# Kernel tuning notes

Measured on AMD Instinct MI355X. Metric: run time of the kernel, lower is better.

## Reference

```python
import jax, jax.numpy as jnp
import numpy as np

N, E, G = 100_000, 1_200_000, 256
EPS = 1e-5

def _bn(a, g, b):
    # BatchNorm1d in training mode: biased batch statistics over dim 0
    mu = a.mean(0)
    var = ((a - mu) ** 2).mean(0)
    return (a - mu) * jax.lax.rsqrt(var + EPS) * g + b

def _cgconv(x, src, dst, ea, Wf, bf, Ws, bs, g, b):
    # PyG CGConv: z = [x_i, x_j, edge_attr]; m = sigmoid(lin_f(z)) * softplus(lin_s(z));
    # out = BN(scatter_add(m -> dst)) + x
    z = jnp.concatenate([x[dst], x[src], ea], axis=-1)      # [E, 2*64+1]
    m = jax.nn.sigmoid(z @ Wf + bf) * jax.nn.softplus(z @ Ws + bs)  # [E, 64]
    agg = jax.ops.segment_sum(m, dst, num_segments=x.shape[0])
    return _bn(agg, g, b) + x

def setup_inputs() -> dict:
    key = jax.random.key(0)
    ks = jax.random.split(key, 16)
    def w(k, shape, scale):
        return jax.random.normal(k, shape, jnp.float32) * scale
    inp = {
        "x": jax.random.normal(ks[0], (N, 12), jnp.float32),
        "edge_index": jax.random.randint(ks[1], (2, E), 0, N, jnp.int32),
        "edge_attr": jax.random.uniform(ks[2], (E, 1), dtype=jnp.float32),
        "batch": jnp.sort(jax.random.randint(ks[3], (N,), 0, G, jnp.int32)),
        "W_in": w(ks[4], (12, 64), 0.3), "b_in": jnp.zeros((64,), jnp.float32),
        "g0": jnp.ones((64,), jnp.float32), "beta0": jnp.zeros((64,), jnp.float32),
    }
    i = 5
    for l in (1, 2, 3):
        inp[f"Wf{l}"] = w(ks[i], (129, 64), 0.1)
        inp[f"bf{l}"] = jnp.zeros((64,), jnp.float32)
        inp[f"Ws{l}"] = w(ks[i + 1], (129, 64), 0.1)
        inp[f"bs{l}"] = jnp.zeros((64,), jnp.float32)
        inp[f"g{l}"] = jnp.ones((64,), jnp.float32)
        inp[f"bb{l}"] = jnp.zeros((64,), jnp.float32)
        i += 2
    inp["W1"] = w(ks[11], (64, 32), 0.15)
    inp["b1"] = jnp.zeros((32,), jnp.float32)
    inp["W2"] = w(ks[12], (32, 1), 0.2)
    inp["b2"] = jnp.zeros((1,), jnp.float32)
    return inp

def reference(x, edge_index, edge_attr, batch,
              W_in, b_in, g0, beta0,
              Wf1, bf1, Ws1, bs1, g1, bb1,
              Wf2, bf2, Ws2, bs2, g2, bb2,
              Wf3, bf3, Ws3, bs3, g3, bb3,
              W1, b1, W2, b2):
    src, dst = edge_index[0], edge_index[1]
    h = jax.nn.relu(_bn(x @ W_in + b_in, g0, beta0))
    h = jax.nn.relu(_cgconv(h, src, dst, edge_attr, Wf1, bf1, Ws1, bs1, g1, bb1))
    h = jax.nn.relu(_cgconv(h, src, dst, edge_attr, Wf2, bf2, Ws2, bs2, g2, bb2))
    h = _cgconv(h, src, dst, edge_attr, Wf3, bf3, Ws3, bs3, g3, bb3)
    # global_mean_pool
    s = jax.ops.segment_sum(h, batch, num_segments=G)
    c = jax.ops.segment_sum(jnp.ones((h.shape[0],), h.dtype), batch, num_segments=G)
    pooled = s / jnp.maximum(c, 1.0)[:, None]
    return jax.nn.relu(pooled @ W1 + b1) @ W2 + b2  # [G, 1]
```

## Files before the change

### kernel.cpp

```cpp
#include <hip/hip_runtime.h>
#include <math.h>

#define N_NODES 100000
#define N_EDGES 1200000
#define N_GRAPHS 256
#define CH 64
#define NC (N_NODES * CH)
#define EPS 1e-5f
#define LOG2E 1.4426950408889634f
#define LN2 0.6931471805599453f
#define EA_SCALE 32768.0f

#define SCAN_NB 98
#define ZSTRN 72
#define GTILES ((N_NODES + 63) / 64)
#define EA_BLOCKS 4096
#define NW (EA_BLOCKS * 4)
#define POOL_BLOCKS 256
#define WP2ROWS 64
#define CAP 48

#define NCOLORS 8
#define SC_BLOCKS 2048
#define NCHUNK (SC_BLOCKS / NCOLORS)
#define CSZ ((N_EDGES + NCHUNK - 1) / NCHUNK)
#define RNODES ((N_NODES + NCOLORS - 1) / NCOLORS)

#define EMB_BLOCKS 512
#define PREP_BLOCKS 192
#define PRE_BLOCKS (SC_BLOCKS + EMB_BLOCKS + PREP_BLOCKS)

typedef _Float16 half8 __attribute__((ext_vector_type(8)));
typedef _Float16 half2v __attribute__((ext_vector_type(2)));
typedef float floatx4 __attribute__((ext_vector_type(4)));

__device__ __forceinline__ int lbound(const int* __restrict__ a, int n, int v) {
    int lo = 0, hi = n;
    while (lo < hi) {
        int mid = (lo + hi) >> 1;
        if (a[mid] < v) lo = mid + 1; else hi = mid;
    }
    return lo;
}

__device__ __forceinline__ float gate2(float f2, float s2) {
    float ef = __builtin_amdgcn_exp2f(-f2);
    float sig = __builtin_amdgcn_rcpf(1.0f + ef);
    float es = __builtin_amdgcn_exp2f(-fabsf(s2));
    float sp = fmaxf(s2, 0.0f) + __builtin_amdgcn_logf(1.0f + es);
    return sig * sp;
}

__global__ void pre_kernel(const int* __restrict__ ei,
                           const float* __restrict__ ea,
                           int* __restrict__ rowptr,
                           unsigned* __restrict__ sef2,
                           const float* __restrict__ x,
                           const float* __restrict__ W,
                           const float* __restrict__ b,
                           _Float16* __restrict__ emb,
                           float* __restrict__ stats,
                           const float* __restrict__ Wf0, const float* __restrict__ Ws0,
                           const float* __restrict__ bf0, const float* __restrict__ bs0,
                           const float* __restrict__ Wf1, const float* __restrict__ Ws1,
                           const float* __restrict__ bf1, const float* __restrict__ bs1,
                           const float* __restrict__ Wf2, const float* __restrict__ Ws2,
                           const float* __restrict__ bf2, const float* __restrict__ bs2,
                           _Float16* __restrict__ WT2,
                           float* __restrict__ w128,
                           float* __restrict__ bias) {
    const int bid = blockIdx.x;
    if (bid < SC_BLOCKS) {
        const int j = bid & (NCOLORS - 1);
        const int k = bid >> 3;
        const int dlo = j * RNODES;
        const int dhi = min(N_NODES, dlo + RNODES);
        const int e0 = k * CSZ;
        const int e1 = min(N_EDGES, e0 + CSZ);
        for (int e = e0 + threadIdx.x; e < e1; e += 256) {
            int d = ei[N_EDGES + e];
            if (d >= dlo && d < dhi) {
                int slot = atomicAdd(&rowptr[d + 1], 1);
                if (slot < CAP) {
                    unsigned v = ((unsigned)ei[e] << 15) | (unsigned)(ea[e] * EA_SCALE);
                    sef2[(size_t)d * CAP + slot] = v;
                }
            }
        }
    } else if (bid < SC_BLOCKS + EMB_BLOCKS) {
        const int eb = bid - SC_BLOCKS;
        int c = threadIdx.x & 63;
        int sub = threadIdx.x >> 6;
        float s = 0.f, q = 0.f;
        for (int r = eb * 4 + sub; r < N_NODES; r += EMB_BLOCKS * 4) {
            const float* xr = x + r * 12;
            float acc = b[c];
#pragma unroll
            for (int k = 0; k < 12; ++k)
                acc = fmaf(xr[k], W[k * CH + c], acc);
            _Float16 h = (_Float16)acc;
            emb[(size_t)r * CH + c] = h;
            float hf = (float)h;
            s += hf;
            q = fmaf(hf, hf, q);
        }
        __shared__ float ls[4][64];
        __shared__ float lq[4][64];
        ls[sub][c] = s;
        lq[sub][c] = q;
        __syncthreads();
        if (sub == 0) {
            s = ls[0][c] + ls[1][c] + ls[2][c] + ls[3][c];
            q = lq[0][c] + lq[1][c] + lq[2][c] + lq[3][c];
            atomicAdd(&stats[c], s);
            atomicAdd(&stats[64 + c], q);
        }
    } else {
        int gid = (bid - SC_BLOCKS - EMB_BLOCKS) * 256 + threadIdx.x;
        int l = gid >> 14;
        int idx = gid & 16383;
        if (l >= 3) return;
        const float* Wf = (l == 0) ? Wf0 : (l == 1) ? Wf1 : Wf2;
        const float* Ws = (l == 0) ? Ws0 : (l == 1) ? Ws1 : Ws2;
        const float* bf = (l == 0) ? bf0 : (l == 1) ? bf1 : bf2;
        const float* bs = (l == 0) ? bs0 : (l == 1) ? bs1 : bs2;
        {
            int cc = idx >> 6;
            int k = idx & 63;
            float v;
            if (cc < 128) {
                int ch = cc >> 1;
                v = (cc & 1) ? Ws[k * 64 + ch] : Wf[k * 64 + ch];
            } else {
                int jj = cc - 128, ch = jj >> 1;
                v = (jj & 1) ? Ws[(64 + k) * 64 + ch] : Wf[(64 + k) * 64 + ch];
            }
            WT2[l * 16384 + idx] = (_Float16)(v * LOG2E);
        }
        if (idx < 128) {
            w128[l * 128 + idx] = ((idx < 64) ? Wf[128 * 64 + idx] : Ws[128 * 64 + (idx - 64)])
                                  * (LOG2E / EA_SCALE);
            bias[l * 128 + idx] = ((idx < 64) ? bf[idx] : bs[idx - 64]) * LOG2E;
        }
    }
}

__global__ void scanA_kernel(int* __restrict__ a, int* __restrict__ btot) {
    __shared__ int wsum[16];
    int t = threadIdx.x, lane = t & 63, w = t >> 6;
    int i = blockIdx.x * 1024 + t;
    int v = (i <= N_NODES) ? a[i] : 0;
    int s = v;
#pragma unroll
    for (int d = 1; d < 64; d <<= 1) {
        int o = __shfl_up(s, d);
        if (lane >= d) s += o;
    }
    if (lane == 63) wsum[w] = s;
    __syncthreads();
    if (w == 0) {
        int ws2 = (lane < 16) ? wsum[lane] : 0;
#pragma unroll
        for (int d = 1; d < 16; d <<= 1) {
            int o = __shfl_up(ws2, d);
            if (lane >= d) ws2 += o;
        }
        if (lane < 16) wsum[lane] = ws2;
    }
    __syncthreads();
    int off = (w > 0) ? wsum[w - 1] : 0;
    if (i <= N_NODES) a[i] = s + off;
    if (t == 0) btot[blockIdx.x] = wsum[15];
}

__global__ void scanB_kernel(int* __restrict__ btot) {
    int lane = threadIdx.x;
    int carry = 0;
    for (int base = 0; base < SCAN_NB; base += 64) {
        int i = base + lane;
        int v = (i < SCAN_NB) ? btot[i] : 0;
        int s = v;
#pragma unroll
        for (int d = 1; d < 64; d <<= 1) {
            int o = __shfl_up(s, d);
            if (lane >= d) s += o;
        }
        if (i < SCAN_NB) btot[i] = s + carry;
        carry += __shfl(s, 63);
    }
}

__global__ void scanC_kernel(int* __restrict__ a, const int* __restrict__ btot) {
    int i = blockIdx.x * 1024 + threadIdx.x;
    int off = (blockIdx.x > 0) ? btot[blockIdx.x - 1] : 0;
    if (i <= N_NODES) a[i] += off;
}

__global__ void wrange_kernel(const int* __restrict__ rowptr,
                              int* __restrict__ wrange) {
    int gid = blockIdx.x * blockDim.x + threadIdx.x;
    if (gid > NW) return;
    if (gid == NW) { wrange[NW] = N_NODES; return; }
    int e0t = (int)((long)gid * N_EDGES / NW);
    wrange[gid] = lbound(rowptr, N_NODES + 1, e0t);
}

template <bool RES, bool RED>
__global__ __launch_bounds__(256)
void node_gemm_kernel(const _Float16* __restrict__ ain,
                      const _Float16* __restrict__ res,
                      const float* __restrict__ stats,
                      const float* __restrict__ gamma,
                      const float* __restrict__ beta,
                      const _Float16* __restrict__ WT2,
                      _Float16* __restrict__ hout,
                      _Float16* __restrict__ pqrs) {
    __shared__ __align__(16) _Float16 As[64 * ZSTRN];
    __shared__ __align__(16) float ab[128];
    __shared__ float sw[128];
    const int t = threadIdx.x;
    const int lane = t & 63;
    const int w = t >> 6;
    const int l15 = lane & 15;
    const int quad = lane >> 4;

    if (RED) {
        if (t < 128) {
            float s = 0.f;
#pragma unroll 8
            for (int r = 0; r < WP2ROWS; ++r) s += stats[r * 128 + t];
            sw[t] = s;
        }
        __syncthreads();
    }
    if (t < 64) {
        float s0 = RED ? sw[t] : stats[t];
        float s1 = RED ? sw[64 + t] : stats[64 + t];
        float mean = s0 * (1.0f / (float)N_NODES);
        float var  = s1 * (1.0f / (float)N_NODES) - mean * mean;
        float inv  = rsqrtf(var + EPS);
        float A = gamma[t] * inv;
        ab[t] = A;
        ab[64 + t] = beta[t] - mean * A;
    }

    half8 bfr[4][2];
#pragma unroll
    for (int tt = 0; tt < 4; ++tt)
#pragma unroll
        for (int ks = 0; ks < 2; ++ks)
            bfr[tt][ks] = *(const half8*)(WT2 + (w * 64 + tt * 16 + l15) * 64 + ks * 32 + quad * 8);
    __syncthreads();

    const int base = blockIdx.x * 64;
    {
        const int e = t >> 2, q = t & 3;
        const int row = base + e;
        const bool valid = (row < N_NODES);
        const int crow = valid ? row : (N_NODES - 1);
        float af[16];
        {
            const _Float16* aph = ain + (size_t)crow * CH + q * 16;
            half8 h0 = *(const half8*)aph;
            half8 h1 = *(const half8*)(aph + 8);
#pragma unroll
            for (int j = 0; j < 8; ++j) { af[j] = (float)h0[j]; af[8 + j] = (float)h1[j]; }
        }
        float rf[16];
        if (RES) {
            const _Float16* rph = res + (size_t)crow * CH + q * 16;
            half8 r0 = *(const half8*)rph;
            half8 r1 = *(const half8*)(rph + 8);
#pragma unroll
            for (int j = 0; j < 8; ++j) { rf[j] = (float)r0[j]; rf[8 + j] = (float)r1[j]; }
        }
        float vv[16];
#pragma unroll
        for (int i = 0; i < 4; ++i) {
            float4 A4 = *(const float4*)(ab + q * 16 + i * 4);
            float4 B4 = *(const float4*)(ab + 64 + q * 16 + i * 4);
#pragma unroll
            for (int jj = 0; jj < 4; ++jj) {
                float Ax = (jj == 0) ? A4.x : (jj == 1) ? A4.y : (jj == 2) ? A4.z : A4.w;
                float Bx = (jj == 0) ? B4.x : (jj == 1) ? B4.y : (jj == 2) ? B4.z : B4.w;
                float r = RES ? rf[i * 4 + jj] : 0.f;
                vv[i * 4 + jj] = fmaxf(fmaf(af[i * 4 + jj], Ax, Bx) + r, 0.0f);
            }
        }
        half8 o0, o1;
#pragma unroll
        for (int j = 0; j < 8; ++j) { o0[j] = (_Float16)vv[j]; o1[j] = (_Float16)vv[8 + j]; }
        *(half8*)(As + e * ZSTRN + q * 16) = o0;
        *(half8*)(As + e * ZSTRN + q * 16 + 8) = o1;
        if (valid) {
            half8* hp = (half8*)(hout + (size_t)row * CH + q * 16);
            hp[0] = o0;
            hp[1] = o1;
        }
    }
    __syncthreads();

    floatx4 acc[4][4];
#pragma unroll
    for (int rt = 0; rt < 4; ++rt)
#pragma unroll
        for (int tt = 0; tt < 4; ++tt)
#pragma unroll
            for (int r = 0; r < 4; ++r) acc[rt][tt][r] = 0.f;

#pragma unroll
    for (int ks = 0; ks < 2; ++ks) {
#pragma unroll
        for (int rt = 0; rt < 4; ++rt) {
            half8 a = *(const half8*)(As + (rt * 16 + l15) * ZSTRN + ks * 32 + quad * 8);
#pragma unroll
            for (int tt = 0; tt < 4; ++tt)
                acc[rt][tt] = __builtin_amdgcn_mfma_f32_16x16x32_f16(a, bfr[tt][ks], acc[rt][tt], 0, 0, 0);
        }
    }

#pragma unroll
    for (int rt = 0; rt < 4; ++rt) {
#pragma unroll
        for (int r = 0; r < 4; ++r) {
            int row = base + rt * 16 + quad * 4 + r;
            if (row < N_NODES) {
#pragma unroll
                for (int tt = 0; tt < 4; ++tt)
                    pqrs[(size_t)row * 256 + w * 64 + tt * 16 + l15] = (_Float16)acc[rt][tt][r];
            }
        }
    }
}

__global__ __launch_bounds__(256)
void edge_agg_kernel(const _Float16* __restrict__ pqrs,
                     const unsigned* __restrict__ sef2,
                     const int* __restrict__ rowptr,
                     const int* __restrict__ wrange,
                     const float* __restrict__ w128,
                     const float* __restrict__ bias,
                     _Float16* __restrict__ agg,
                     float* __restrict__ wpart2) {
    const int lane = threadIdx.x & 63;
    const int w = threadIdx.x >> 6;
    const int gw = __builtin_amdgcn_readfirstlane(blockIdx.x * 4 + w);
    const float wfc = w128[lane], wsc = w128[64 + lane];
    const float bfc = bias[lane], bsc = bias[64 + lane];
    const half2v* __restrict__ prb = (const half2v*)pqrs;
    const half2v* __restrict__ qsb = (const half2v*)pqrs + 64;

    const int n0 = wrange[gw];
    const int n1 = wrange[gw + 1];

    float ssum = 0.f, sqsum = 0.f;
    if (n0 < n1) {
        half2v prn = prb[(size_t)n0 * 128 + lane];
        int rp1 = rowptr[n0];
        for (int n = n0; n < n1; ++n) {
            const int rp0 = rp1;
            rp1 = rowptr[n + 1];
            int deg = rp1 - rp0;
            if (deg > CAP) deg = CAP;
            const unsigned* sp = sef2 + (size_t)n * CAP;
            half2v pr = prn;
            {
                int np = (n + 1 < N_NODES) ? (n + 1) : (N_NODES - 1);
                prn = prb[(size_t)np * 128 + lane];
            }
            const float fb = (float)pr[0] + bfc;
            const float sb = (float)pr[1] + bsc;
            float acc0 = 0.f, acc1 = 0.f, acc2 = 0.f, acc3 = 0.f;
            int e = 0;
            for (; e + 8 <= deg; e += 8) {
                unsigned s0 = sp[e],     s1 = sp[e + 1], s2 = sp[e + 2], s3 = sp[e + 3];
                unsigned s4 = sp[e + 4], s5 = sp[e + 5], s6 = sp[e + 6], s7 = sp[e + 7];
                half2v q0 = qsb[(size_t)(s0 >> 15) * 128 + lane];
                half2v q1 = qsb[(size_t)(s1 >> 15) * 128 + lane];
                half2v q2 = qsb[(size_t)(s2 >> 15) * 128 + lane];
                half2v q3 = qsb[(size_t)(s3 >> 15) * 128 + lane];
                half2v q4 = qsb[(size_t)(s4 >> 15) * 128 + lane];
                half2v q5 = qsb[(size_t)(s5 >> 15) * 128 + lane];
                half2v q6 = qsb[(size_t)(s6 >> 15) * 128 + lane];
                half2v q7 = qsb[(size_t)(s7 >> 15) * 128 + lane];
                float ea0 = (float)(s0 & 32767u), ea1 = (float)(s1 & 32767u);
                float ea2 = (float)(s2 & 32767u), ea3 = (float)(s3 & 32767u);
                float ea4 = (float)(s4 & 32767u), ea5 = (float)(s5 & 32767u);
                float ea6 = (float)(s6 & 32767u), ea7 = (float)(s7 & 32767u);
                acc0 += gate2(fmaf(ea0, wfc, fb + (float)q0[0]), fmaf(ea0, wsc, sb + (float)q0[1]));
                acc1 += gate2(fmaf(ea1, wfc, fb + (float)q1[0]), fmaf(ea1, wsc, sb + (float)q1[1]));
                acc2 += gate2(fmaf(ea2, wfc, fb + (float)q2[0]), fmaf(ea2, wsc, sb + (float)q2[1]));
                acc3 += gate2(fmaf(ea3, wfc, fb + (float)q3[0]), fmaf(ea3, wsc, sb + (float)q3[1]));
                acc0 += gate2(fmaf(ea4, wfc, fb + (float)q4[0]), fmaf(ea4, wsc, sb + (float)q4[1]));
                acc1 += gate2(fmaf(ea5, wfc, fb + (float)q5[0]), fmaf(ea5, wsc, sb + (float)q5[1]));
                acc2 += gate2(fmaf(ea6, wfc, fb + (float)q6[0]), fmaf(ea6, wsc, sb + (float)q6[1]));
                acc3 += gate2(fmaf(ea7, wfc, fb + (float)q7[0]), fmaf(ea7, wsc, sb + (float)q7[1]));
            }
            if (e + 4 <= deg) {
                unsigned s0 = sp[e], s1 = sp[e + 1], s2 = sp[e + 2], s3 = sp[e + 3];
                half2v q0 = qsb[(size_t)(s0 >> 15) * 128 + lane];
                half2v q1 = qsb[(size_t)(s1 >> 15) * 128 + lane];
                half2v q2 = qsb[(size_t)(s2 >> 15) * 128 + lane];
                half2v q3 = qsb[(size_t)(s3 >> 15) * 128 + lane];
                float ea0 = (float)(s0 & 32767u), ea1 = (float)(s1 & 32767u);
                float ea2 = (float)(s2 & 32767u), ea3 = (float)(s3 & 32767u);
                acc0 += gate2(fmaf(ea0, wfc, fb + (float)q0[0]), fmaf(ea0, wsc, sb + (float)q0[1]));
                acc1 += gate2(fmaf(ea1, wfc, fb + (float)q1[0]), fmaf(ea1, wsc, sb + (float)q1[1]));
                acc2 += gate2(fmaf(ea2, wfc, fb + (float)q2[0]), fmaf(ea2, wsc, sb + (float)q2[1]));
                acc3 += gate2(fmaf(ea3, wfc, fb + (float)q3[0]), fmaf(ea3, wsc, sb + (float)q3[1]));
                e += 4;
            }
            for (; e < deg; ++e) {
                unsigned s0 = sp[e];
                half2v q0 = qsb[(size_t)(s0 >> 15) * 128 + lane];
                float ea0 = (float)(s0 & 32767u);
                acc0 += gate2(fmaf(ea0, wfc, fb + (float)q0[0]), fmaf(ea0, wsc, sb + (float)q0[1]));
            }
            _Float16 ah = (_Float16)(LN2 * ((acc0 + acc1) + (acc2 + acc3)));
            agg[(size_t)n * CH + lane] = ah;
            float acc = (float)ah;
            ssum += acc;
            sqsum = fmaf(acc, acc, sqsum);
        }
    }
    __shared__ float reds[4][128];
    reds[w][lane] = ssum;
    reds[w][64 + lane] = sqsum;
    __syncthreads();
    if (w == 0) {
        float a = reds[0][lane] + reds[1][lane] + reds[2][lane] + reds[3][lane];
        float b = reds[0][64 + lane] + reds[1][64 + lane] + reds[2][64 + lane] + reds[3][64 + lane];
        float* wp = wpart2 + (size_t)(blockIdx.x & (WP2ROWS - 1)) * 128;
        atomicAdd(&wp[lane], a);
        atomicAdd(&wp[64 + lane], b);
    }
}

__global__ __launch_bounds__(256)
void pool_bn_kernel(const _Float16* __restrict__ ain,
                    const _Float16* __restrict__ res,
                    const float* __restrict__ wp2,
                    const float* __restrict__ gamma,
                    const float* __restrict__ beta,
                    const int* __restrict__ batch,
                    float* __restrict__ pooled,
                    float* __restrict__ counts) {
    __shared__ float sw[128];
    __shared__ float ab[128];
    if (threadIdx.x < 128) {
        float s = 0.f;
#pragma unroll 8
        for (int r = 0; r < WP2ROWS; ++r) s += wp2[r * 128 + threadIdx.x];
        sw[threadIdx.x] = s;
    }
    __syncthreads();
    if (threadIdx.x < 64) {
        int t = threadIdx.x;
        float mean = sw[t] * (1.0f / (float)N_NODES);
        float var  = sw[64 + t] * (1.0f / (float)N_NODES) - mean * mean;
        float inv  = rsqrtf(var + EPS);
        float A = gamma[t] * inv;
        ab[t] = A;
        ab[64 + t] = beta[t] - mean * A;
    }
    __syncthreads();

    const int c = threadIdx.x & 63;
    const float A = ab[c], B = ab[64 + c];
    const int walker = blockIdx.x * 4 + (threadIdx.x >> 6);
    const int nwalk = POOL_BLOCKS * 4;
    const int chunk = (N_NODES + nwalk - 1) / nwalk;
    int r0 = walker * chunk;
    int r1 = min(N_NODES, r0 + chunk);
    if (r0 >= r1) return;

    int cur = batch[r0];
    float acc = 0.0f;
    int runlen = 0;
    for (int r = r0; r < r1; ++r) {
        int b = batch[r];
        if (b != cur) {
            atomicAdd(&pooled[cur * CH + c], acc);
            if (c == 0) atomicAdd(&counts[cur], (float)runlen);
            acc = 0.0f;
            runlen = 0;
            cur = b;
        }
        size_t idx = (size_t)r * CH + c;
        acc += fmaf((float)ain[idx], A, B) + (float)res[idx];
        ++runlen;
    }
    atomicAdd(&pooled[cur * CH + c], acc);
    if (c == 0) atomicAdd(&counts[cur], (float)runlen);
}

__global__ void head_kernel(const float* __restrict__ pooled,
                            const float* __restrict__ counts,
                            const float* __restrict__ W1,
                            const float* __restrict__ b1,
                            const float* __restrict__ W2,
                            const float* __restrict__ b2,
                            float* __restrict__ out) {
    int gph = blockIdx.x;
    int t = threadIdx.x;
    __shared__ float p[64];
    __shared__ float h1[32];
    float cnt = fmaxf(counts[gph], 1.0f);
    p[t] = pooled[gph * CH + t] / cnt;
    __syncthreads();
    if (t < 32) {
        float acc = b1[t];
#pragma unroll
        for (int c = 0; c < 64; ++c)
            acc = fmaf(p[c], W1[c * 32 + t], acc);
        h1[t] = fmaxf(acc, 0.0f);
    }
    __syncthreads();
    if (t == 0) {
        float acc = b2[0];
#pragma unroll
        for (int j = 0; j < 32; ++j)
            acc = fmaf(h1[j], W2[j], acc);
        out[gph] = acc;
    }
}

extern "C" void kernel_launch(void* const* d_in, const int* in_sizes, int n_in,
                              void* d_out, int out_size, void* d_ws, size_t ws_size,
                              hipStream_t stream) {
    const float* x     = (const float*)d_in[0];
    const int*   ei    = (const int*)d_in[1];
    const float* ea    = (const float*)d_in[2];
    const int*   batch = (const int*)d_in[3];
    const float* W_in  = (const float*)d_in[4];
    const float* b_in  = (const float*)d_in[5];
    const float* g0    = (const float*)d_in[6];
    const float* beta0 = (const float*)d_in[7];

    const float* Wf[3] = {(const float*)d_in[8],  (const float*)d_in[14], (const float*)d_in[20]};
    const float* bfv[3]= {(const float*)d_in[9],  (const float*)d_in[15], (const float*)d_in[21]};
    const float* Wsv[3]= {(const float*)d_in[10], (const float*)d_in[16], (const float*)d_in[22]};
    const float* bsv[3]= {(const float*)d_in[11], (const float*)d_in[17], (const float*)d_in[23]};
    const float* gm[3] = {(const float*)d_in[12], (const float*)d_in[18], (const float*)d_in[24]};
    const float* bb[3] = {(const float*)d_in[13], (const float*)d_in[19], (const float*)d_in[25]};

    const float* W1 = (const float*)d_in[26];
    const float* b1 = (const float*)d_in[27];
    const float* W2 = (const float*)d_in[28];
    const float* b2 = (const float*)d_in[29];

    float* out = (float*)d_out;

#define ALIGN256(v) (((v) + 255) & ~(size_t)255)
    char* base = (char*)d_ws;
    size_t off = 0;
    _Float16* bufA = (_Float16*)(base + off); off = ALIGN256(off + (size_t)NC * 2);
    _Float16* bufB = (_Float16*)(base + off); off = ALIGN256(off + (size_t)NC * 2);
    _Float16* AGG = (_Float16*)(base + off);  off = ALIGN256(off + (size_t)NC * 2);
    _Float16* WT2 = (_Float16*)(base + off);  off = ALIGN256(off + 3 * 256 * 64 * 2);
    float* w128   = (float*)(base + off);     off = ALIGN256(off + 3 * 128 * 4);
    float* biasL  = (float*)(base + off);     off = ALIGN256(off + 3 * 128 * 4);
    unsigned* sef2 = (unsigned*)(base + off); off = ALIGN256(off + (size_t)N_NODES * CAP * 4);
    _Float16* pqrs = (_Float16*)(base + off); off = ALIGN256(off + (size_t)N_NODES * 256 * 2);
    int* wrange   = (int*)(base + off);       off = ALIGN256(off + (size_t)(NW + 1) * 4);
    char* zbase   = base + off;
    int* rowptr   = (int*)(base + off);       off = ALIGN256(off + (size_t)(N_NODES + 1) * 4);
    int* btot     = (int*)(base + off);       off = ALIGN256(off + SCAN_NB * 4);
    float* stats0 = (float*)(base + off);     off = ALIGN256(off + 128 * 4);
    float* wpart2 = (float*)(base + off);     off = ALIGN256(off + 3 * WP2ROWS * 128 * 4);
    float* pooled = (float*)(base + off);     off = ALIGN256(off + (size_t)N_GRAPHS * CH * 4);
    float* counts = (float*)(base + off);     off = ALIGN256(off + (size_t)N_GRAPHS * 4);
    size_t zbytes = (size_t)(base + off - zbase);

    hipMemsetAsync(zbase, 0, zbytes, stream);

    pre_kernel<<<PRE_BLOCKS, 256, 0, stream>>>(
        ei, ea, rowptr, sef2, x, W_in, b_in, bufA, stats0,
        Wf[0], Wsv[0], bfv[0], bsv[0],
        Wf[1], Wsv[1], bfv[1], bsv[1],
        Wf[2], Wsv[2], bfv[2], bsv[2],
        WT2, w128, biasL);

    scanA_kernel<<<SCAN_NB, 1024, 0, stream>>>(rowptr, btot);
    scanB_kernel<<<1, 64, 0, stream>>>(btot);
    scanC_kernel<<<SCAN_NB, 1024, 0, stream>>>(rowptr, btot);
    wrange_kernel<<<(NW + 256) / 256, 256, 0, stream>>>(rowptr, wrange);

    node_gemm_kernel<false, false><<<GTILES, 256, 0, stream>>>(
        bufA, nullptr, stats0, g0, beta0, WT2 + 0 * 256 * 64, bufB, pqrs);
    edge_agg_kernel<<<EA_BLOCKS, 256, 0, stream>>>(
        pqrs, sef2, rowptr, wrange, w128 + 0 * 128, biasL + 0 * 128, AGG,
        wpart2 + 0 * WP2ROWS * 128);

    node_gemm_kernel<true, true><<<GTILES, 256, 0, stream>>>(
        AGG, bufB, wpart2 + 0 * WP2ROWS * 128, gm[0], bb[0], WT2 + 1 * 256 * 64, bufA, pqrs);
    edge_agg_kernel<<<EA_BLOCKS, 256, 0, stream>>>(
        pqrs, sef2, rowptr, wrange, w128 + 1 * 128, biasL + 1 * 128, AGG,
        wpart2 + 1 * WP2ROWS * 128);

    node_gemm_kernel<true, true><<<GTILES, 256, 0, stream>>>(
        AGG, bufA, wpart2 + 1 * WP2ROWS * 128, gm[1], bb[1], WT2 + 2 * 256 * 64, bufB, pqrs);
    edge_agg_kernel<<<EA_BLOCKS, 256, 0, stream>>>(
        pqrs, sef2, rowptr, wrange, w128 + 2 * 128, biasL + 2 * 128, AGG,
        wpart2 + 2 * WP2ROWS * 128);

    pool_bn_kernel<<<POOL_BLOCKS, 256, 0, stream>>>(
        AGG, bufB, wpart2 + 2 * WP2ROWS * 128, gm[2], bb[2], batch, pooled, counts);
    head_kernel<<<N_GRAPHS, 64, 0, stream>>>(pooled, counts, W1, b1, W2, b2, out);
}
```

Baseline: 512.2 us.

## Drop rowptr scan and wrange search; split node ranges evenly and stage edge scatter in LDS

The three-kernel prefix scan and the binary-search work-range kernel are removed. Edge aggregation now gives each wave an even slice of nodes and reads per-node degree counts directly, so four launches leave the critical path. The scatter in pre_kernel first queues matching edges in shared memory, then flushes them with global atomics on per-node counters. Splitting by node count instead of edge count can unbalance work across waves, and the LDS staging adds barriers and shared memory to every block of the fused pre_kernel.

```diff
diff --git a/kernel.cpp b/kernel.cpp
--- a/kernel.cpp
+++ b/kernel.cpp
@@ -11,7 +11,6 @@
 #define LN2 0.6931471805599453f
 #define EA_SCALE 32768.0f
 
-#define SCAN_NB 98
 #define ZSTRN 72
 #define GTILES ((N_NODES + 63) / 64)
 #define EA_BLOCKS 4096
@@ -19,6 +18,7 @@
 #define POOL_BLOCKS 256
 #define WP2ROWS 64
 #define CAP 48
+#define LDSQ 1024
 
 #define NCOLORS 8
 #define SC_BLOCKS 2048
@@ -33,15 +33,6 @@
 typedef _Float16 half8 __attribute__((ext_vector_type(8)));
 typedef _Float16 half2v __attribute__((ext_vector_type(2)));
 typedef float floatx4 __attribute__((ext_vector_type(4)));
-
-__device__ __forceinline__ int lbound(const int* __restrict__ a, int n, int v) {
-    int lo = 0, hi = n;
-    while (lo < hi) {
-        int mid = (lo + hi) >> 1;
-        if (a[mid] < v) lo = mid + 1; else hi = mid;
-    }
-    return lo;
-}
 
 __device__ __forceinline__ float gate2(float f2, float s2) {
     float ef = __builtin_amdgcn_exp2f(-f2);
@@ -53,7 +44,7 @@
 
 __global__ void pre_kernel(const int* __restrict__ ei,
                            const float* __restrict__ ea,
-                           int* __restrict__ rowptr,
+                           int* __restrict__ cnt,
                            unsigned* __restrict__ sef2,
                            const float* __restrict__ x,
                            const float* __restrict__ W,
@@ -69,8 +60,13 @@
                            _Float16* __restrict__ WT2,
                            float* __restrict__ w128,
                            float* __restrict__ bias) {
+    __shared__ int lcnt;
+    __shared__ int ldst[LDSQ];
+    __shared__ unsigned lpay[LDSQ];
     const int bid = blockIdx.x;
     if (bid < SC_BLOCKS) {
+        if (threadIdx.x == 0) lcnt = 0;
+        __syncthreads();
         const int j = bid & (NCOLORS - 1);
         const int k = bid >> 3;
         const int dlo = j * RNODES;
@@ -80,12 +76,21 @@
         for (int e = e0 + threadIdx.x; e < e1; e += 256) {
             int d = ei[N_EDGES + e];
             if (d >= dlo && d < dhi) {
-                int slot = atomicAdd(&rowptr[d + 1], 1);
-                if (slot < CAP) {
-                    unsigned v = ((unsigned)ei[e] << 15) | (unsigned)(ea[e] * EA_SCALE);
-                    sef2[(size_t)d * CAP + slot] = v;
+                unsigned v = ((unsigned)ei[e] << 15) | (unsigned)(ea[e] * EA_SCALE);
+                int i = atomicAdd(&lcnt, 1);
+                if (i < LDSQ) { ldst[i] = d; lpay[i] = v; }
+                else {
+                    int slot = atomicAdd(&cnt[d], 1);
+                    if (slot < CAP) sef2[(size_t)d * CAP + slot] = v;
                 }
             }
+        }
+        __syncthreads();
+        const int m = min(lcnt, LDSQ);
+        for (int i = threadIdx.x; i < m; i += 256) {
+            int d = ldst[i];
+            int slot = atomicAdd(&cnt[d], 1);
+            if (slot < CAP) sef2[(size_t)d * CAP + slot] = lpay[i];
         }
     } else if (bid < SC_BLOCKS + EMB_BLOCKS) {
         const int eb = bid - SC_BLOCKS;
@@ -145,66 +150,6 @@
     }
 }
 
-__global__ void scanA_kernel(int* __restrict__ a, int* __restrict__ btot) {
-    __shared__ int wsum[16];
-    int t = threadIdx.x, lane = t & 63, w = t >> 6;
-    int i = blockIdx.x * 1024 + t;
-    int v = (i <= N_NODES) ? a[i] : 0;
-    int s = v;
-#pragma unroll
-    for (int d = 1; d < 64; d <<= 1) {
-        int o = __shfl_up(s, d);
-        if (lane >= d) s += o;
-    }
-    if (lane == 63) wsum[w] = s;
-    __syncthreads();
-    if (w == 0) {
-        int ws2 = (lane < 16) ? wsum[lane] : 0;
-#pragma unroll
-        for (int d = 1; d < 16; d <<= 1) {
-            int o = __shfl_up(ws2, d);
-            if (lane >= d) ws2 += o;
-        }
-        if (lane < 16) wsum[lane] = ws2;
-    }
-    __syncthreads();
-    int off = (w > 0) ? wsum[w - 1] : 0;
-    if (i <= N_NODES) a[i] = s + off;
-    if (t == 0) btot[blockIdx.x] = wsum[15];
-}
-
-__global__ void scanB_kernel(int* __restrict__ btot) {
-    int lane = threadIdx.x;
-    int carry = 0;
-    for (int base = 0; base < SCAN_NB; base += 64) {
-        int i = base + lane;
-        int v = (i < SCAN_NB) ? btot[i] : 0;
-        int s = v;
-#pragma unroll
-        for (int d = 1; d < 64; d <<= 1) {
-            int o = __shfl_up(s, d);
-            if (lane >= d) s += o;
-        }
-        if (i < SCAN_NB) btot[i] = s + carry;
-        carry += __shfl(s, 63);
-    }
-}
-
-__global__ void scanC_kernel(int* __restrict__ a, const int* __restrict__ btot) {
-    int i = blockIdx.x * 1024 + threadIdx.x;
-    int off = (blockIdx.x > 0) ? btot[blockIdx.x - 1] : 0;
-    if (i <= N_NODES) a[i] += off;
-}
-
-__global__ void wrange_kernel(const int* __restrict__ rowptr,
-                              int* __restrict__ wrange) {
-    int gid = blockIdx.x * blockDim.x + threadIdx.x;
-    if (gid > NW) return;
-    if (gid == NW) { wrange[NW] = N_NODES; return; }
-    int e0t = (int)((long)gid * N_EDGES / NW);
-    wrange[gid] = lbound(rowptr, N_NODES + 1, e0t);
-}
-
 template <bool RES, bool RED>
 __global__ __launch_bounds__(256)
 void node_gemm_kernel(const _Float16* __restrict__ ain,
@@ -336,8 +281,7 @@
 __global__ __launch_bounds__(256)
 void edge_agg_kernel(const _Float16* __restrict__ pqrs,
                      const unsigned* __restrict__ sef2,
-                     const int* __restrict__ rowptr,
-                     const int* __restrict__ wrange,
+                     const int* __restrict__ cnt,
                      const float* __restrict__ w128,
                      const float* __restrict__ bias,
                      _Float16* __restrict__ agg,
@@ -350,17 +294,14 @@
     const half2v* __restrict__ prb = (const half2v*)pqrs;
     const half2v* __restrict__ qsb = (const half2v*)pqrs + 64;
 
-    const int n0 = wrange[gw];
-    const int n1 = wrange[gw + 1];
+    const int n0 = (int)((long)gw * N_NODES / NW);
+    const int n1 = (int)((long)(gw + 1) * N_NODES / NW);
 
     float ssum = 0.f, sqsum = 0.f;
     if (n0 < n1) {
         half2v prn = prb[(size_t)n0 * 128 + lane];
-        int rp1 = rowptr[n0];
         for (int n = n0; n < n1; ++n) {
-            const int rp0 = rp1;
-            rp1 = rowptr[n + 1];
-            int deg = rp1 - rp0;
+            int deg = cnt[n];
             if (deg > CAP) deg = CAP;
             const unsigned* sp = sef2 + (size_t)n * CAP;
             half2v pr = prn;
@@ -562,10 +503,8 @@
     float* biasL  = (float*)(base + off);     off = ALIGN256(off + 3 * 128 * 4);
     unsigned* sef2 = (unsigned*)(base + off); off = ALIGN256(off + (size_t)N_NODES * CAP * 4);
     _Float16* pqrs = (_Float16*)(base + off); off = ALIGN256(off + (size_t)N_NODES * 256 * 2);
-    int* wrange   = (int*)(base + off);       off = ALIGN256(off + (size_t)(NW + 1) * 4);
     char* zbase   = base + off;
-    int* rowptr   = (int*)(base + off);       off = ALIGN256(off + (size_t)(N_NODES + 1) * 4);
-    int* btot     = (int*)(base + off);       off = ALIGN256(off + SCAN_NB * 4);
+    int* cnt      = (int*)(base + off);       off = ALIGN256(off + (size_t)N_NODES * 4);
     float* stats0 = (float*)(base + off);     off = ALIGN256(off + 128 * 4);
     float* wpart2 = (float*)(base + off);     off = ALIGN256(off + 3 * WP2ROWS * 128 * 4);
     float* pooled = (float*)(base + off);     off = ALIGN256(off + (size_t)N_GRAPHS * CH * 4);
@@ -575,33 +514,28 @@
     hipMemsetAsync(zbase, 0, zbytes, stream);
 
     pre_kernel<<<PRE_BLOCKS, 256, 0, stream>>>(
-        ei, ea, rowptr, sef2, x, W_in, b_in, bufA, stats0,
+        ei, ea, cnt, sef2, x, W_in, b_in, bufA, stats0,
         Wf[0], Wsv[0], bfv[0], bsv[0],
         Wf[1], Wsv[1], bfv[1], bsv[1],
         Wf[2], Wsv[2], bfv[2], bsv[2],
         WT2, w128, biasL);
 
-    scanA_kernel<<<SCAN_NB, 1024, 0, stream>>>(rowptr, btot);
-    scanB_kernel<<<1, 64, 0, stream>>>(btot);
-    scanC_kernel<<<SCAN_NB, 1024, 0, stream>>>(rowptr, btot);
-    wrange_kernel<<<(NW + 256) / 256, 256, 0, stream>>>(rowptr, wrange);
-
     node_gemm_kernel<false, false><<<GTILES, 256, 0, stream>>>(
         bufA, nullptr, stats0, g0, beta0, WT2 + 0 * 256 * 64, bufB, pqrs);
     edge_agg_kernel<<<EA_BLOCKS, 256, 0, stream>>>(
-        pqrs, sef2, rowptr, wrange, w128 + 0 * 128, biasL + 0 * 128, AGG,
+        pqrs, sef2, cnt, w128 + 0 * 128, biasL + 0 * 128, AGG,
         wpart2 + 0 * WP2ROWS * 128);
 
     node_gemm_kernel<true, true><<<GTILES, 256, 0, stream>>>(
         AGG, bufB, wpart2 + 0 * WP2ROWS * 128, gm[0], bb[0], WT2 + 1 * 256 * 64, bufA, pqrs);
     edge_agg_kernel<<<EA_BLOCKS, 256, 0, stream>>>(
-        pqrs, sef2, rowptr, wrange, w128 + 1 * 128, biasL + 1 * 128, AGG,
+        pqrs, sef2, cnt, w128 + 1 * 128, biasL + 1 * 128, AGG,
         wpart2 + 1 * WP2ROWS * 128);
 
     node_gemm_kernel<true, true><<<GTILES, 256, 0, stream>>>(
         AGG, bufA, wpart2 + 1 * WP2ROWS * 128, gm[1], bb[1], WT2 + 2 * 256 * 64, bufB, pqrs);
     edge_agg_kernel<<<EA_BLOCKS, 256, 0, stream>>>(
-        pqrs, sef2, rowptr, wrange, w128 + 2 * 128, biasL + 2 * 128, AGG,
+        pqrs, sef2, cnt, w128 + 2 * 128, biasL + 2 * 128, AGG,
         wpart2 + 2 * WP2ROWS * 128);
 
     pool_bn_kernel<<<POOL_BLOCKS, 256, 0, stream>>>(
```

Result: faster. 499.0 us (median of 2 runs) (-2.6%).
